# Kernel optimization log

Measured on AMD Instinct MI355X. Metric: run time of the kernel, lower is better.

The kernel has to match this reference:

```python
import jax, jax.numpy as jnp
import numpy as np
from jax import lax

T, B, F = 512, 256, 258
IN, H = 256, 1024


def setup_inputs() -> dict:
    key = jax.random.key(0)
    ks = jax.random.split(key, 6)

    def lin_w(k, fi, fo):
        return jax.random.normal(k, (fi, fo), jnp.float32) * (1.0 / np.sqrt(fi))

    return {
        "u": jax.random.normal(ks[0], (T, B, F), jnp.float32),
        "a": jnp.float32(0.92),
        "b": jnp.float32(-0.3),
        "W0": lin_w(ks[1], IN, H), "b0": jnp.zeros((H,), jnp.float32),
        "W1": lin_w(ks[2], H, H), "b1": jnp.zeros((H,), jnp.float32),
        "W2": lin_w(ks[3], H, H), "b2": jnp.zeros((H,), jnp.float32),
        "W3": lin_w(ks[4], H, 1), "b3": jnp.zeros((1,), jnp.float32),
    }


def reference(u, a, b, W0, b0, W1, b1, W2, b2, W3, b3):
    Tn, Bn, Fn = u.shape
    # MLP over cols 2: — independent of the recurrent state, so batch all timesteps.
    feats = u[:, :, 2:].reshape(Tn * Bn, Fn - 2)
    h = jax.nn.relu(feats @ W0 + b0)
    h = jax.nn.relu(h @ W1 + b1)
    h = jax.nn.relu(h @ W2 + b2)
    net = (h @ W3 + b3).reshape(Tn, Bn)  # [T, B]

    c1 = u[:, :, 1]  # [T, B], multiplied by b each step
    y0 = u[0, :, 0]  # u_y[0]; also the col-0 value used at j=0

    def step(carry, xs):
        net_j, c1_j = xs
        y = a * carry + b * c1_j + net_j
        return y, y

    _, ys = lax.scan(step, y0, (net, c1))  # ys: [T, B] = u_y[1:]
    return jnp.concatenate([y0[None, :], ys], axis=0)  # [T+1, B]
```

## Files before the change

### kernel.cpp

```cpp
#include <hip/hip_runtime.h>
#include <hip/hip_fp16.h>

typedef _Float16 v8h __attribute__((ext_vector_type(8)));
typedef _Float16 v4h __attribute__((ext_vector_type(4)));
typedef float v4f __attribute__((ext_vector_type(4)));

#define T_DIM 512
#define B_DIM 256
#define F_DIM 258
#define IN_DIM 256
#define H_DIM 1024
#define M_ROWS (T_DIM * B_DIM)

__device__ __forceinline__ void tile_map(int b, int nM, int nN, int& mt, int& nt) {
    if ((nM & 7) == 0) {
        int xcd = b & 7;
        int l = b >> 3;
        int mpx = nM >> 3;
        int lm = l / nN;
        mt = xcd * mpx + lm;
        nt = l - lm * nN;
    } else {
        int lm = b / nN;
        mt = lm;
        nt = b - lm * nN;
    }
}

__device__ __forceinline__ void gl16(const _Float16* g, _Float16* l) {
    __builtin_amdgcn_global_load_lds(
        (const __attribute__((address_space(1))) unsigned int*)g,
        (__attribute__((address_space(3))) unsigned int*)l, 16, 0, 0);
}


__global__ void prep_u_kernel(const float* __restrict__ u,
                              _Float16* __restrict__ X,
                              float* __restrict__ c1, int n) {
    int i = blockIdx.x * blockDim.x + threadIdx.x;
    int stride = gridDim.x * blockDim.x;
    for (; i < n; i += stride) {
        float v = u[i];
        unsigned r = (unsigned)i / 258u;
        unsigned c = (unsigned)i - r * 258u;
        if (c >= 2u) {
            unsigned k = c - 2u;
            X[((r >> 4) * 32u + (k >> 3)) * 128u + (r & 15u) * 8u + (k & 7u)] =
                (_Float16)v;
        } else if (c == 1u) {
            c1[r] = v;
        }
    }
}

__global__ void wt_frag_kernel(const float* __restrict__ W,
                               _Float16* __restrict__ BF, int K, int N) {
    int idx = blockIdx.x * blockDim.x + threadIdx.x;
    int total = (N >> 6) * (K >> 5) * 4 * 64;
    if (idx >= total) return;
    int l = idx & 63;
    int f = idx >> 6;
    int i = f & 3;
    int gk = f >> 2;
    int KC = K >> 5;
    int g = gk / KC, kc = gk - g * KC;
    int col = g * 64 + i * 16 + (l & 15);
    int krow = kc * 32 + (l >> 4) * 8;
    _Float16 tmp[8];
#pragma unroll
    for (int j = 0; j < 8; ++j) tmp[j] = (_Float16)W[(size_t)(krow + j) * N + col];
    *(v8h*)&BF[(size_t)idx * 8] = *(v8h*)tmp;
}

__global__ void wt_vec_kernel(const float* __restrict__ W,
                              _Float16* __restrict__ Wh, int K) {
    int i = blockIdx.x * blockDim.x + threadIdx.x;
    if (i < K) Wh[i] = (_Float16)W[i];
}

__global__ void zero_kernel(float* __restrict__ p, int n) {
    int i = blockIdx.x * blockDim.x + threadIdx.x;
    if (i < n) p[i] = 0.f;
}

template <int MI0>
__device__ __forceinline__ void mfma_pair(v4f (&acc)[8][4], const v8h (&af)[4][2],
                                          v8h b00, v8h b01, v8h b10, v8h b11) {
#pragma unroll
    for (int ni = 0; ni < 4; ++ni) {
        acc[MI0][ni] = __builtin_amdgcn_mfma_f32_16x16x32_f16(
            af[ni][0], b00, acc[MI0][ni], 0, 0, 0);
        acc[MI0][ni] = __builtin_amdgcn_mfma_f32_16x16x32_f16(
            af[ni][1], b01, acc[MI0][ni], 0, 0, 0);
        acc[MI0 + 1][ni] = __builtin_amdgcn_mfma_f32_16x16x32_f16(
            af[ni][0], b10, acc[MI0 + 1][ni], 0, 0, 0);
        acc[MI0 + 1][ni] = __builtin_amdgcn_mfma_f32_16x16x32_f16(
            af[ni][1], b11, acc[MI0 + 1][ni], 0, 0, 0);
    }
}

template <int DOT>
__global__ __launch_bounds__(512, 2)
void gemm256(const _Float16* __restrict__ Xb, const _Float16* __restrict__ WF,
             const float* __restrict__ bias, const _Float16* __restrict__ w3,
             _Float16* __restrict__ Cb, float* __restrict__ net,
             int M, int N, int K) {
    extern __shared__ _Float16 lds[];
    const int tid = threadIdx.x;
    const int lane = tid & 63;
    const int wave = tid >> 6;
    const int wm = wave >> 2;
    const int wn = wave & 3;
    const int quad = lane >> 4;
    const int r16 = lane & 15;
    const int wm8 = wm * 8;
    const int lrb = (lane >> 4) * 128 + r16 * 8;

    int mt, nt;
    tile_map(blockIdx.x, M >> 8, N >> 8, mt, nt);
    const int m0 = mt * 256;
    const int n0 = nt * 256;

    const int KC = K >> 5;
    const int KC8 = K >> 3;
    const int NT = K >> 6;
    const int m016 = m0 >> 4;
    const int nt4 = nt * 4;

    auto stageA = [&](int g, int kt, _Float16* pa) {
        gl16(WF + ((size_t)(nt4 + g) * KC + (size_t)kt * 2) * 2048 + tid * 8,
             pa + g * 4096 + tid * 8);
    };
    auto stageB = [&](int mb, int kt, _Float16* pb) {
        gl16(Xb + ((size_t)(m016 + mb + (tid >> 7)) * KC8 + (size_t)kt * 8) * 128 +
                 (tid & 127) * 8,
             pb + mb * 1024 + tid * 8);
    };

    v4f acc[8][4];
#pragma unroll
    for (int i = 0; i < 8; ++i)
#pragma unroll
        for (int j = 0; j < 4; ++j) acc[i][j] = (v4f)0.f;

    {
        _Float16* A0 = lds;
        _Float16* B0 = lds + 16384;
        stageB(0, 0, B0); stageB(8, 0, B0);
        stageA(0, 0, A0); stageA(1, 0, A0); stageA(2, 0, A0); stageA(3, 0, A0);
        stageB(4, 0, B0); stageB(12, 0, B0);
        asm volatile("s_waitcnt vmcnt(2)" ::: "memory");
        __builtin_amdgcn_s_barrier();
    }

#pragma unroll 2
    for (int kt = 0; kt < NT; ++kt) {
        _Float16* pAc = lds + (kt & 1) * 32768;
        _Float16* pBc = pAc + 16384;
        _Float16* pAn = lds + ((kt + 1) & 1) * 32768;
        _Float16* pBn = pAn + 16384;
        const bool pre = (kt + 1 < NT);
        const int kn = kt + 1;

        v8h af[4][2];

        {
#pragma unroll
            for (int i = 0; i < 4; ++i) {
                af[i][0] = *(const v8h*)(pAc + wn * 4096 + i * 512 + lane * 8);
                af[i][1] = *(const v8h*)(pAc + wn * 4096 + (4 + i) * 512 + lane * 8);
            }
            v8h b00 = *(const v8h*)(pBc + (wm8 + 0) * 1024 + lrb);
            v8h b01 = *(const v8h*)(pBc + (wm8 + 0) * 1024 + 512 + lrb);
            v8h b10 = *(const v8h*)(pBc + (wm8 + 1) * 1024 + lrb);
            v8h b11 = *(const v8h*)(pBc + (wm8 + 1) * 1024 + 512 + lrb);
            if (pre) { stageB(0, kn, pBn); stageB(8, kn, pBn); }
            __builtin_amdgcn_s_barrier();
            __builtin_amdgcn_s_setprio(1);
            mfma_pair<0>(acc, af, b00, b01, b10, b11);
            __builtin_amdgcn_s_setprio(0);
            __builtin_amdgcn_s_barrier();
        }
        {
            v8h b00 = *(const v8h*)(pBc + (wm8 + 2) * 1024 + lrb);
            v8h b01 = *(const v8h*)(pBc + (wm8 + 2) * 1024 + 512 + lrb);
            v8h b10 = *(const v8h*)(pBc + (wm8 + 3) * 1024 + lrb);
            v8h b11 = *(const v8h*)(pBc + (wm8 + 3) * 1024 + 512 + lrb);
            if (pre) { stageA(0, kn, pAn); stageA(1, kn, pAn); }
            __builtin_amdgcn_s_barrier();
            __builtin_amdgcn_s_setprio(1);
            mfma_pair<2>(acc, af, b00, b01, b10, b11);
            __builtin_amdgcn_s_setprio(0);
            if (pre)
                asm volatile("s_waitcnt vmcnt(4)" ::: "memory");
            else
                asm volatile("s_waitcnt vmcnt(0)" ::: "memory");
            __builtin_amdgcn_s_barrier();
        }
        {
            v8h b00 = *(const v8h*)(pBc + (wm8 + 4) * 1024 + lrb);
            v8h b01 = *(const v8h*)(pBc + (wm8 + 4) * 1024 + 512 + lrb);
            v8h b10 = *(const v8h*)(pBc + (wm8 + 5) * 1024 + lrb);
            v8h b11 = *(const v8h*)(pBc + (wm8 + 5) * 1024 + 512 + lrb);
            if (pre) { stageA(2, kn, pAn); stageA(3, kn, pAn); }
            __builtin_amdgcn_s_barrier();
            __builtin_amdgcn_s_setprio(1);
            mfma_pair<4>(acc, af, b00, b01, b10, b11);
            __builtin_amdgcn_s_setprio(0);
            __builtin_amdgcn_s_barrier();
        }
        {
            v8h b00 = *(const v8h*)(pBc + (wm8 + 6) * 1024 + lrb);
            v8h b01 = *(const v8h*)(pBc + (wm8 + 6) * 1024 + 512 + lrb);
            v8h b10 = *(const v8h*)(pBc + (wm8 + 7) * 1024 + lrb);
            v8h b11 = *(const v8h*)(pBc + (wm8 + 7) * 1024 + 512 + lrb);
            if (pre) { stageB(4, kn, pBn); stageB(12, kn, pBn); }
            __builtin_amdgcn_s_barrier();
            __builtin_amdgcn_s_setprio(1);
            mfma_pair<6>(acc, af, b00, b01, b10, b11);
            __builtin_amdgcn_s_setprio(0);
            if (pre) asm volatile("s_waitcnt vmcnt(2)" ::: "memory");
            __builtin_amdgcn_s_barrier();
        }
    }

    const int nb = n0 + wn * 64;
    v4f bv[4];
#pragma unroll
    for (int ni = 0; ni < 4; ++ni)
        bv[ni] = *(const v4f*)&bias[nb + ni * 16 + quad * 4];

    if constexpr (DOT == 0) {
        const int NC8 = N >> 3;
#pragma unroll
        for (int ni = 0; ni < 4; ++ni) {
            const int nblk = ((nb + ni * 16) >> 3) + (quad >> 1);
#pragma unroll
            for (int mi = 0; mi < 8; ++mi) {
                v4h hv;
#pragma unroll
                for (int i = 0; i < 4; ++i)
                    hv[i] = (_Float16)fmaxf(acc[mi][ni][i] + bv[ni][i], 0.f);
                const size_t mblk = (size_t)((m0 + wm * 128 + mi * 16) >> 4);
                _Float16* dst =
                    Cb + (mblk * NC8 + nblk) * 128 + r16 * 8 + (quad & 1) * 4;
                *(v4h*)dst = hv;
            }
        }
    } else {
        v4h wv[4];
#pragma unroll
        for (int ni = 0; ni < 4; ++ni)
            wv[ni] = *(const v4h*)&w3[nb + ni * 16 + quad * 4];
#pragma unroll
        for (int mi = 0; mi < 8; ++mi) {
            float t = 0.f;
#pragma unroll
            for (int ni = 0; ni < 4; ++ni)
#pragma unroll
                for (int i = 0; i < 4; ++i) {
                    float v = fmaxf(acc[mi][ni][i] + bv[ni][i], 0.f);
                    t = fmaf(v, (float)wv[ni][i], t);
                }
            t += __shfl_xor(t, 16);
            t += __shfl_xor(t, 32);
            if (quad == 0) {
                int row = m0 + wm * 128 + mi * 16 + r16;
                atomicAdd(&net[row], t);
            }
        }
    }
}

__global__ void scan_kernel(const float* __restrict__ net,
                            const float* __restrict__ c1,
                            const float* __restrict__ u,
                            const float* __restrict__ pa,
                            const float* __restrict__ pb,
                            const float* __restrict__ pb3,
                            float* __restrict__ out) {
    const int bidx = threadIdx.x;
    const float a = pa[0];
    const float b = pb[0];
    const float b3 = pb3[0];
    float y = u[(size_t)bidx * F_DIM];
    out[bidx] = y;
#pragma unroll 8
    for (int t = 0; t < T_DIM; ++t) {
        float z = fmaf(b, c1[t * B_DIM + bidx], net[t * B_DIM + bidx] + b3);
        y = fmaf(a, y, z);
        out[(t + 1) * B_DIM + bidx] = y;
    }
}

extern "C" void kernel_launch(void* const* d_in, const int* in_sizes, int n_in,
                              void* d_out, int out_size, void* d_ws, size_t ws_size,
                              hipStream_t stream) {
    const float* u = (const float*)d_in[0];
    const float* pa = (const float*)d_in[1];
    const float* pb = (const float*)d_in[2];
    const float* W0 = (const float*)d_in[3];
    const float* b0 = (const float*)d_in[4];
    const float* W1 = (const float*)d_in[5];
    const float* b1 = (const float*)d_in[6];
    const float* W2 = (const float*)d_in[7];
    const float* b2 = (const float*)d_in[8];
    const float* W3 = (const float*)d_in[9];
    const float* b3 = (const float*)d_in[10];
    float* out = (float*)d_out;

    char* ws = (char*)d_ws;
    size_t off = 0;
    auto alloc = [&](size_t bytes) -> void* {
        void* p = ws + off;
        off += (bytes + 255) & ~(size_t)255;
        return p;
    };

    float* net = (float*)alloc((size_t)M_ROWS * 4);
    float* c1 = (float*)alloc((size_t)M_ROWS * 4);
    _Float16* W0F = (_Float16*)alloc((size_t)IN_DIM * H_DIM * 2);
    _Float16* W1F = (_Float16*)alloc((size_t)H_DIM * H_DIM * 2);
    _Float16* W2F = (_Float16*)alloc((size_t)H_DIM * H_DIM * 2);
    _Float16* W3h = (_Float16*)alloc((size_t)H_DIM * 2);

    const size_t per_row = 512 + 2048 + 2048;
    size_t avail = (ws_size > off + 65536) ? (ws_size - off - 65536) : 0;
    long Rl = (long)(avail / per_row);
    Rl = (Rl / 2048) * 2048;
    if (Rl < 2048) Rl = 2048;
    if (Rl > M_ROWS) Rl = M_ROWS;
    const int R = (int)Rl;

    _Float16* Xc = (_Float16*)alloc((size_t)R * IN_DIM * 2);
    _Float16* HAc = (_Float16*)alloc((size_t)R * H_DIM * 2);
    _Float16* HBc = (_Float16*)alloc((size_t)R * H_DIM * 2);

    wt_frag_kernel<<<(IN_DIM / 32) * (H_DIM / 64), 256, 0, stream>>>(W0, W0F,
                                                                     IN_DIM, H_DIM);
    wt_frag_kernel<<<(H_DIM / 32) * (H_DIM / 64), 256, 0, stream>>>(W1, W1F,
                                                                    H_DIM, H_DIM);
    wt_frag_kernel<<<(H_DIM / 32) * (H_DIM / 64), 256, 0, stream>>>(W2, W2F,
                                                                    H_DIM, H_DIM);
    wt_vec_kernel<<<4, 256, 0, stream>>>(W3, W3h, H_DIM);
    zero_kernel<<<M_ROWS / 256, 256, 0, stream>>>(net, M_ROWS);

    const size_t lds_bytes = 131072;
    for (int r0 = 0; r0 < M_ROWS; r0 += R) {
        int Mc = M_ROWS - r0;
        if (Mc > R) Mc = R;
        int nElem = Mc * F_DIM;
        int pgrid = (nElem + 256 * 8 - 1) / (256 * 8);
        if (pgrid > 2048) pgrid = 2048;
        prep_u_kernel<<<pgrid, 256, 0, stream>>>(u + (size_t)r0 * F_DIM, Xc,
                                                 c1 + r0, nElem);

        dim3 blk(512);
        dim3 grd((Mc / 256) * (H_DIM / 256));
        gemm256<0><<<grd, blk, lds_bytes, stream>>>(Xc, W0F, b0, nullptr, HAc,
                                                    nullptr, Mc, H_DIM, IN_DIM);
        gemm256<0><<<grd, blk, lds_bytes, stream>>>(HAc, W1F, b1, nullptr, HBc,
                                                    nullptr, Mc, H_DIM, H_DIM);
        gemm256<1><<<grd, blk, lds_bytes, stream>>>(HBc, W2F, b2, W3h, nullptr,
                                                    net + r0, Mc, H_DIM, H_DIM);
    }

    scan_kernel<<<1, 256, 0, stream>>>(net, c1, u, pa, pb, b3, out);
}
```

Before: 946.3 us.

## Replace four-phase barrier pipeline with single-barrier loop and double-buffered LDS fragments

Each K-iteration previously ran four phases, each with two workgroup barriers and interleaved global-to-LDS staging. Now all next-tile global loads are issued at once at the start of the iteration, B fragments are read from LDS into two alternating register sets one phase ahead of the MFMAs that use them, and one wait plus one barrier closes the iteration. This removes about seven barriers per iteration and should let LDS reads overlap MFMA work, at the cost of more registers held live, bursty global traffic, and a full vmcnt(0) drain every iteration.

```diff
diff --git a/kernel.cpp b/kernel.cpp
--- a/kernel.cpp
+++ b/kernel.cpp
@@ -85,17 +85,17 @@
 
 template <int MI0>
 __device__ __forceinline__ void mfma_pair(v4f (&acc)[8][4], const v8h (&af)[4][2],
-                                          v8h b00, v8h b01, v8h b10, v8h b11) {
+                                          const v8h (&b)[4]) {
 #pragma unroll
     for (int ni = 0; ni < 4; ++ni) {
         acc[MI0][ni] = __builtin_amdgcn_mfma_f32_16x16x32_f16(
-            af[ni][0], b00, acc[MI0][ni], 0, 0, 0);
+            af[ni][0], b[0], acc[MI0][ni], 0, 0, 0);
         acc[MI0][ni] = __builtin_amdgcn_mfma_f32_16x16x32_f16(
-            af[ni][1], b01, acc[MI0][ni], 0, 0, 0);
+            af[ni][1], b[1], acc[MI0][ni], 0, 0, 0);
         acc[MI0 + 1][ni] = __builtin_amdgcn_mfma_f32_16x16x32_f16(
-            af[ni][0], b10, acc[MI0 + 1][ni], 0, 0, 0);
+            af[ni][0], b[2], acc[MI0 + 1][ni], 0, 0, 0);
         acc[MI0 + 1][ni] = __builtin_amdgcn_mfma_f32_16x16x32_f16(
-            af[ni][1], b11, acc[MI0 + 1][ni], 0, 0, 0);
+            af[ni][1], b[3], acc[MI0 + 1][ni], 0, 0, 0);
     }
 }
 
@@ -136,6 +136,12 @@
                  (tid & 127) * 8,
              pb + mb * 1024 + tid * 8);
     };
+    auto loadB = [&](const _Float16* pB, int mb, v8h (&b)[4]) {
+        b[0] = *(const v8h*)(pB + mb * 1024 + lrb);
+        b[1] = *(const v8h*)(pB + mb * 1024 + 512 + lrb);
+        b[2] = *(const v8h*)(pB + (mb + 1) * 1024 + lrb);
+        b[3] = *(const v8h*)(pB + (mb + 1) * 1024 + 512 + lrb);
+    };
 
     v4f acc[8][4];
 #pragma unroll
@@ -146,10 +152,9 @@
     {
         _Float16* A0 = lds;
         _Float16* B0 = lds + 16384;
-        stageB(0, 0, B0); stageB(8, 0, B0);
+        stageB(0, 0, B0); stageB(4, 0, B0); stageB(8, 0, B0); stageB(12, 0, B0);
         stageA(0, 0, A0); stageA(1, 0, A0); stageA(2, 0, A0); stageA(3, 0, A0);
-        stageB(4, 0, B0); stageB(12, 0, B0);
-        asm volatile("s_waitcnt vmcnt(2)" ::: "memory");
+        asm volatile("s_waitcnt vmcnt(0)" ::: "memory");
         __builtin_amdgcn_s_barrier();
     }
 
@@ -163,63 +168,43 @@
         const int kn = kt + 1;
 
         v8h af[4][2];
-
-        {
-#pragma unroll
-            for (int i = 0; i < 4; ++i) {
-                af[i][0] = *(const v8h*)(pAc + wn * 4096 + i * 512 + lane * 8);
-                af[i][1] = *(const v8h*)(pAc + wn * 4096 + (4 + i) * 512 + lane * 8);
-            }
-            v8h b00 = *(const v8h*)(pBc + (wm8 + 0) * 1024 + lrb);
-            v8h b01 = *(const v8h*)(pBc + (wm8 + 0) * 1024 + 512 + lrb);
-            v8h b10 = *(const v8h*)(pBc + (wm8 + 1) * 1024 + lrb);
-            v8h b11 = *(const v8h*)(pBc + (wm8 + 1) * 1024 + 512 + lrb);
-            if (pre) { stageB(0, kn, pBn); stageB(8, kn, pBn); }
-            __builtin_amdgcn_s_barrier();
-            __builtin_amdgcn_s_setprio(1);
-            mfma_pair<0>(acc, af, b00, b01, b10, b11);
-            __builtin_amdgcn_s_setprio(0);
-            __builtin_amdgcn_s_barrier();
-        }
-        {
-            v8h b00 = *(const v8h*)(pBc + (wm8 + 2) * 1024 + lrb);
-            v8h b01 = *(const v8h*)(pBc + (wm8 + 2) * 1024 + 512 + lrb);
-            v8h b10 = *(const v8h*)(pBc + (wm8 + 3) * 1024 + lrb);
-            v8h b11 = *(const v8h*)(pBc + (wm8 + 3) * 1024 + 512 + lrb);
-            if (pre) { stageA(0, kn, pAn); stageA(1, kn, pAn); }
-            __builtin_amdgcn_s_barrier();
-            __builtin_amdgcn_s_setprio(1);
-            mfma_pair<2>(acc, af, b00, b01, b10, b11);
-            __builtin_amdgcn_s_setprio(0);
-            if (pre)
-                asm volatile("s_waitcnt vmcnt(4)" ::: "memory");
-            else
-                asm volatile("s_waitcnt vmcnt(0)" ::: "memory");
-            __builtin_amdgcn_s_barrier();
-        }
-        {
-            v8h b00 = *(const v8h*)(pBc + (wm8 + 4) * 1024 + lrb);
-            v8h b01 = *(const v8h*)(pBc + (wm8 + 4) * 1024 + 512 + lrb);
-            v8h b10 = *(const v8h*)(pBc + (wm8 + 5) * 1024 + lrb);
-            v8h b11 = *(const v8h*)(pBc + (wm8 + 5) * 1024 + 512 + lrb);
-            if (pre) { stageA(2, kn, pAn); stageA(3, kn, pAn); }
-            __builtin_amdgcn_s_barrier();
-            __builtin_amdgcn_s_setprio(1);
-            mfma_pair<4>(acc, af, b00, b01, b10, b11);
-            __builtin_amdgcn_s_setprio(0);
-            __builtin_amdgcn_s_barrier();
-        }
-        {
-            v8h b00 = *(const v8h*)(pBc + (wm8 + 6) * 1024 + lrb);
-            v8h b01 = *(const v8h*)(pBc + (wm8 + 6) * 1024 + 512 + lrb);
-            v8h b10 = *(const v8h*)(pBc + (wm8 + 7) * 1024 + lrb);
-            v8h b11 = *(const v8h*)(pBc + (wm8 + 7) * 1024 + 512 + lrb);
-            if (pre) { stageB(4, kn, pBn); stageB(12, kn, pBn); }
-            __builtin_amdgcn_s_barrier();
-            __builtin_amdgcn_s_setprio(1);
-            mfma_pair<6>(acc, af, b00, b01, b10, b11);
-            __builtin_amdgcn_s_setprio(0);
-            if (pre) asm volatile("s_waitcnt vmcnt(2)" ::: "memory");
+#pragma unroll
+        for (int i = 0; i < 4; ++i) {
+            af[i][0] = *(const v8h*)(pAc + wn * 4096 + i * 512 + lane * 8);
+            af[i][1] = *(const v8h*)(pAc + wn * 4096 + (4 + i) * 512 + lane * 8);
+        }
+        v8h bA[4], bB[4];
+        loadB(pBc, wm8 + 0, bA);
+
+        if (pre) {
+            stageB(0, kn, pBn); stageB(4, kn, pBn);
+            stageB(8, kn, pBn); stageB(12, kn, pBn);
+            stageA(0, kn, pAn); stageA(1, kn, pAn);
+            stageA(2, kn, pAn); stageA(3, kn, pAn);
+        }
+
+        loadB(pBc, wm8 + 2, bB);
+        __builtin_amdgcn_s_setprio(1);
+        mfma_pair<0>(acc, af, bA);
+        __builtin_amdgcn_s_setprio(0);
+
+        loadB(pBc, wm8 + 4, bA);
+        __builtin_amdgcn_s_setprio(1);
+        mfma_pair<2>(acc, af, bB);
+        __builtin_amdgcn_s_setprio(0);
+
+        loadB(pBc, wm8 + 6, bB);
+        __builtin_amdgcn_s_setprio(1);
+        mfma_pair<4>(acc, af, bA);
+        __builtin_amdgcn_s_setprio(0);
+
+        __builtin_amdgcn_s_setprio(1);
+        mfma_pair<6>(acc, af, bB);
+        __builtin_amdgcn_s_setprio(0);
+
+        if (kt != NT - 1) {
+            asm volatile("s_waitcnt lgkmcnt(0)" ::: "memory");
+            asm volatile("s_waitcnt vmcnt(0)" ::: "memory");
             __builtin_amdgcn_s_barrier();
         }
     }
```

Result: no change. 937.0 us (-1.0%).
